# Kernel tuning notes

Hardware: AMD Instinct MI355X
Metric: run time of the kernel (lower is better)

Reference implementation:

```python
import jax, jax.numpy as jnp
import numpy as np

D_MODEL = 1024
VOCAB = 32000
NUM_HEADS = 3  # MTP steps
NHEAD = 2      # attention heads per encoder layer
D_FF = 2048    # torch TransformerEncoderLayer default dim_feedforward
EPS_RMS = 1e-8
EPS_LN = 1e-5


def rmsnorm(x):
    rms = jnp.sqrt(jnp.mean(x * x, axis=-1, keepdims=True) + EPS_RMS)
    return x / rms


def layernorm(x, g, b):
    m = jnp.mean(x, axis=-1, keepdims=True)
    v = jnp.mean((x - m) ** 2, axis=-1, keepdims=True)
    return (x - m) / jnp.sqrt(v + EPS_LN) * g + b


def encoder_layer_single_token(x, p):
    # x: (..., d). Self-attention over a length-1 sequence: softmax over one key
    # gives attention weight 1, so attn_out = Wo @ (Wv @ x). Post-norm (torch default).
    v = x @ p['Wv'].T + p['bv']
    attn = v @ p['Wo'].T + p['bo']
    x = layernorm(x + attn, p['ln1_g'], p['ln1_b'])
    ff = jax.nn.relu(x @ p['W1'].T + p['b1']) @ p['W2'].T + p['b2']
    x = layernorm(x + ff, p['ln2_g'], p['ln2_b'])
    return x


def setup_inputs() -> dict:
    key = jax.random.key(0)
    ks = jax.random.split(key, 4)
    token_ids = jax.random.randint(ks[0], (4, 512), 0, VOCAB)
    embed = jax.random.normal(ks[1], (VOCAB, D_MODEL), dtype=jnp.float32) * 0.02
    s = 1.0 / np.sqrt(D_MODEL)
    params = []
    kk = ks[2]
    for k in range(NUM_HEADS):
        kk, *sub = jax.random.split(kk, 10)
        p = {
            'Wmerge': jax.random.normal(sub[0], (D_MODEL, 2 * D_MODEL)) * s,
            'bmerge': jnp.zeros((D_MODEL,)),
            'Wv': jax.random.normal(sub[1], (D_MODEL, D_MODEL)) * s,
            'bv': jnp.zeros((D_MODEL,)),
            'Wo': jax.random.normal(sub[2], (D_MODEL, D_MODEL)) * s,
            'bo': jnp.zeros((D_MODEL,)),
            'W1': jax.random.normal(sub[3], (D_FF, D_MODEL)) * s,
            'b1': jnp.zeros((D_FF,)),
            'W2': jax.random.normal(sub[4], (D_MODEL, D_FF)) * (1.0 / np.sqrt(D_FF)),
            'b2': jnp.zeros((D_MODEL,)),
            'ln1_g': jnp.ones((D_MODEL,)), 'ln1_b': jnp.zeros((D_MODEL,)),
            'ln2_g': jnp.ones((D_MODEL,)), 'ln2_b': jnp.zeros((D_MODEL,)),
        }
        params.append(p)
    # flatten params into dict entries layer{k}_{name}
    out = {'token_ids': token_ids, 'embed': embed}
    for k, p in enumerate(params):
        for name, val in p.items():
            out[f'l{k}_{name}'] = val
    return out


def _forward(token_ids, embed, layers):
    B, T = token_ids.shape
    embeds = embed[token_ids]              # (B, T, d)
    n_pos = T - NUM_HEADS                  # positions i = 0 .. T-NUM_HEADS-1
    # vectorize over i: h_prev starts as h0_seq[:, i, :] for all i at once
    idx = jnp.arange(n_pos)
    h_prev = embeds[:, idx, :]             # (B, P, d)
    logits_list = []
    for k in range(NUM_HEADS):
        p = layers[k]
        tok = embeds[:, idx + (k + 1), :]  # (B, P, d) future token embeds
        merged = jnp.concatenate([rmsnorm(h_prev), rmsnorm(tok)], axis=-1)  # (B,P,2d)
        x = merged @ p['Wmerge'].T + p['bmerge']                            # (B,P,d)
        h_curr = encoder_layer_single_token(x, p)
        logits = h_curr @ embed.T          # tied unembed (B,P,V)
        logits_list.append(logits)
        h_prev = h_curr
    # stack -> (B, P, NUM_HEADS, V) matching torch stack(dim=1) per-position then outer list
    return jnp.stack(logits_list, axis=2)


def reference(token_ids, embed,
              l0_Wmerge, l0_bmerge, l0_Wv, l0_bv, l0_Wo, l0_bo, l0_W1, l0_b1, l0_W2, l0_b2, l0_ln1_g, l0_ln1_b, l0_ln2_g, l0_ln2_b,
              l1_Wmerge, l1_bmerge, l1_Wv, l1_bv, l1_Wo, l1_bo, l1_W1, l1_b1, l1_W2, l1_b2, l1_ln1_g, l1_ln1_b, l1_ln2_g, l1_ln2_b,
              l2_Wmerge, l2_bmerge, l2_Wv, l2_bv, l2_Wo, l2_bo, l2_W1, l2_b1, l2_W2, l2_b2, l2_ln1_g, l2_ln1_b, l2_ln2_g, l2_ln2_b):
    names = ['Wmerge', 'bmerge', 'Wv', 'bv', 'Wo', 'bo', 'W1', 'b1', 'W2', 'b2', 'ln1_g', 'ln1_b', 'ln2_g', 'ln2_b']
    vals = [l0_Wmerge, l0_bmerge, l0_Wv, l0_bv, l0_Wo, l0_bo, l0_W1, l0_b1, l0_W2, l0_b2, l0_ln1_g, l0_ln1_b, l0_ln2_g, l0_ln2_b,
            l1_Wmerge, l1_bmerge, l1_Wv, l1_bv, l1_Wo, l1_bo, l1_W1, l1_b1, l1_W2, l1_b2, l1_ln1_g, l1_ln1_b, l1_ln2_g, l1_ln2_b,
            l2_Wmerge, l2_bmerge, l2_Wv, l2_bv, l2_Wo, l2_bo, l2_W1, l2_b1, l2_W2, l2_b2, l2_ln1_g, l2_ln1_b, l2_ln2_g, l2_ln2_b]
    layers = [dict(zip(names, vals[i * 14:(i + 1) * 14])) for i in range(NUM_HEADS)]
    return _forward(token_ids, embed, layers)
```

## Files before the change

kernel.cpp:

```cpp
#include <hip/hip_runtime.h>


#define NPOS   509
#define MROWS  2036
#define MPAD   2048
#define DMODEL 1024

typedef _Float16 f16;
typedef _Float16 f16x8 __attribute__((ext_vector_type(8)));
typedef _Float16 f16x4 __attribute__((ext_vector_type(4)));
typedef float    f32x4 __attribute__((ext_vector_type(4)));

#define MFMA16(a, b, c) __builtin_amdgcn_mfma_f32_16x16x32_f16(a, b, c, 0, 0, 0)
#define VM0   asm volatile("s_waitcnt vmcnt(0)" ::: "memory")
#define VM2   asm volatile("s_waitcnt vmcnt(2)" ::: "memory")
#define VM4   asm volatile("s_waitcnt vmcnt(4)" ::: "memory")
#define LGKM0 asm volatile("s_waitcnt lgkmcnt(0)" ::: "memory")
#define SCHED0 __builtin_amdgcn_sched_barrier(0)
#define BAR   asm volatile("s_barrier" ::: "memory")

__device__ __forceinline__ void gld_lds16(const void* g, void* l) {
  __builtin_amdgcn_global_load_lds(
      (const __attribute__((address_space(1))) void*)g,
      (__attribute__((address_space(3))) void*)l, 16, 0, 0);
}

__global__ __launch_bounds__(256) void conv_f32_f16(const float* __restrict__ src,
                                                    f16* __restrict__ dst, long n) {
  long i = ((long)blockIdx.x * 256 + threadIdx.x) * 8;
  if (i + 8 <= n) {
    float4 a = *(const float4*)(src + i);
    float4 b = *(const float4*)(src + i + 4);
    f16x8 o = {(f16)a.x, (f16)a.y, (f16)a.z, (f16)a.w,
               (f16)b.x, (f16)b.y, (f16)b.z, (f16)b.w};
    *(f16x8*)(dst + i) = o;
  }
}

struct ConvArgs { const float* s[12]; f16* d[12]; long n[12]; };
__global__ __launch_bounds__(256) void conv_many(ConvArgs a) {
  int t = blockIdx.y;
  long i = ((long)blockIdx.x * 256 + threadIdx.x) * 8;
  if (i + 8 <= a.n[t]) {
    const float* src = a.s[t];
    float4 x = *(const float4*)(src + i);
    float4 y = *(const float4*)(src + i + 4);
    f16x8 o = {(f16)x.x, (f16)x.y, (f16)x.z, (f16)x.w,
               (f16)y.x, (f16)y.y, (f16)y.z, (f16)y.w};
    *(f16x8*)(a.d[t] + i) = o;
  }
}

struct TpArgs { const float* s[3]; f16* d[3]; };
__global__ __launch_bounds__(256) void transpose3(TpArgs a) {
  __shared__ float t[32][33];
  int h = blockIdx.z;
  int bx = blockIdx.x * 32, by = blockIdx.y * 32;
  int tx = threadIdx.x & 31, ty = threadIdx.x >> 5;
  const float* src = a.s[h];
  f16* dst = a.d[h];
  #pragma unroll
  for (int r = 0; r < 32; r += 8)
    t[ty + r][tx] = src[(long)(by + ty + r) * 1024 + bx + tx];
  __syncthreads();
  #pragma unroll
  for (int r = 0; r < 32; r += 8)
    dst[(long)(bx + ty + r) * 1024 + by + tx] = (f16)t[tx][ty + r];
}

struct BvoArgs { const float* Wo[3]; const float* bv[3]; const float* bo[3]; float* out[3]; };
__global__ __launch_bounds__(64) void make_bvo3(BvoArgs a) {
  int h = blockIdx.y, r = blockIdx.x, l = threadIdx.x;
  const float* Wo = a.Wo[h];
  const float* bv = a.bv[h];
  float s = 0.0f;
  for (int k = l; k < 1024; k += 64) s += Wo[(long)r * 1024 + k] * bv[k];
  #pragma unroll
  for (int off = 32; off > 0; off >>= 1) s += __shfl_xor(s, off);
  if (l == 0) a.out[h][r] = s + a.bo[h][r];
}

__device__ __forceinline__ float2 block_reduce2(float a, float b) {
  #pragma unroll
  for (int off = 32; off > 0; off >>= 1) {
    a += __shfl_xor(a, off);
    b += __shfl_xor(b, off);
  }
  __shared__ float2 red[4];
  int wv = threadIdx.x >> 6;
  if ((threadIdx.x & 63) == 0) red[wv] = make_float2(a, b);
  __syncthreads();
  float2 r0 = red[0], r1 = red[1], r2 = red[2], r3 = red[3];
  return make_float2(r0.x + r1.x + r2.x + r3.x, r0.y + r1.y + r2.y + r3.y);
}

__global__ __launch_bounds__(256) void merge_rms(const float* __restrict__ hprev,
                                                 const float* __restrict__ embed,
                                                 const int* __restrict__ tok,
                                                 f16* __restrict__ merged, int koff,
                                                 int hsel) {
  int r = blockIdx.x;
  int b = r / NPOS, t = r - b * NPOS;
  int tid = threadIdx.x;
  const float* hrow = (hsel >= 0)
      ? embed + (long)tok[b * 512 + t + hsel] * DMODEL
      : hprev + (long)r * DMODEL;
  float4 hv = ((const float4*)hrow)[tid];
  float4 tv = ((const float4*)(embed + (long)tok[b * 512 + t + koff] * DMODEL))[tid];
  float sh = hv.x * hv.x + hv.y * hv.y + hv.z * hv.z + hv.w * hv.w;
  float st = tv.x * tv.x + tv.y * tv.y + tv.z * tv.z + tv.w * tv.w;
  float2 tot = block_reduce2(sh, st);
  float ih = 1.0f / sqrtf(tot.x * (1.0f / DMODEL) + 1e-8f);
  float it = 1.0f / sqrtf(tot.y * (1.0f / DMODEL) + 1e-8f);
  f16x4 oh = {(f16)(hv.x * ih), (f16)(hv.y * ih), (f16)(hv.z * ih), (f16)(hv.w * ih)};
  f16x4 ot = {(f16)(tv.x * it), (f16)(tv.y * it), (f16)(tv.z * it), (f16)(tv.w * it)};
  *(f16x4*)(merged + (long)r * 2048 + tid * 4) = oh;
  *(f16x4*)(merged + (long)r * 2048 + 1024 + tid * 4) = ot;
}

__global__ __launch_bounds__(256) void add_ln(const float* __restrict__ x,
                                              const float* __restrict__ res,
                                              const float* __restrict__ g,
                                              const float* __restrict__ bb,
                                              float* __restrict__ yf,
                                              f16* __restrict__ yh) {
  int r = blockIdx.x, tid = threadIdx.x;
  float4 a = ((const float4*)(x + (long)r * DMODEL))[tid];
  float4 c = ((const float4*)(res + (long)r * DMODEL))[tid];
  a.x += c.x; a.y += c.y; a.z += c.z; a.w += c.w;
  float s  = a.x + a.y + a.z + a.w;
  float ss = a.x * a.x + a.y * a.y + a.z * a.z + a.w * a.w;
  float2 tot = block_reduce2(s, ss);
  float mean = tot.x * (1.0f / DMODEL);
  float var  = tot.y * (1.0f / DMODEL) - mean * mean;
  float inv  = 1.0f / sqrtf(var + 1e-5f);
  float4 gv = ((const float4*)g)[tid];
  float4 bv = ((const float4*)bb)[tid];
  float y0 = (a.x - mean) * inv * gv.x + bv.x;
  float y1 = (a.y - mean) * inv * gv.y + bv.y;
  float y2 = (a.z - mean) * inv * gv.z + bv.z;
  float y3 = (a.w - mean) * inv * gv.w + bv.w;
  float4 o = {y0, y1, y2, y3};
  ((float4*)(yf + (long)r * DMODEL))[tid] = o;
  f16x4 oh = {(f16)y0, (f16)y1, (f16)y2, (f16)y3};
  *(f16x4*)(yh + (long)r * DMODEL + tid * 4) = oh;
}

template <int HAS_BIAS, int RELU, int WF32, int WF16, int MASK>
__global__ __launch_bounds__(256) void gemm_sm(const f16* __restrict__ A,
                                               const f16* __restrict__ B,
                                               const float* __restrict__ bias,
                                               float* __restrict__ Cf,
                                               f16* __restrict__ Ch,
                                               int K, int N, long ldc, long coff,
                                               int mval, long zsA, long zsB, long zsC) {
  __shared__ __align__(16) f16 sA[3][2048];
  __shared__ __align__(16) f16 sB[3][2048];
  const int tid  = threadIdx.x;
  const int lane = tid & 63, wv = tid >> 6;
  const int wm = wv >> 1, wn = wv & 1;
  const int bm = blockIdx.y, bn = blockIdx.x;
  const int lr = lane & 15, lk = lane >> 4;

  A += (long)blockIdx.z * zsA;
  B += (long)blockIdx.z * zsB;
  Ch += (long)blockIdx.z * zsC;

  const f16* gA = A + ((long)(bm * 64 + (tid >> 2))) * K + (tid & 3) * 8;
  const f16* gB = B + ((long)(bn * 64 + (tid >> 2))) * K + (tid & 3) * 8;

  const int aoff = (wm * 32 + lr) * 32 + lk * 8;
  const int boff = (wn * 32 + lr) * 32 + lk * 8;

  f32x4 acc[2][2] = {};

#define SSTAGE(buf, kt)                                \
  gld_lds16(gA + (long)(kt) * 32, &sA[buf][tid * 8]);  \
  gld_lds16(gB + (long)(kt) * 32, &sB[buf][tid * 8]);

  const int nk = K >> 5;
  SSTAGE(0, 0);
  SSTAGE(1, 1);

  int cur = 0, stg = 2;
  for (int kt = 0; kt < nk; ++kt) {
    if (kt + 1 < nk) { VM2; } else { VM0; }
    BAR;
    if (kt + 2 < nk) { SSTAGE(stg, kt + 2); }
    f16x8 af0 = *(const f16x8*)&sA[cur][aoff];
    f16x8 af1 = *(const f16x8*)&sA[cur][aoff + 512];
    f16x8 bf0 = *(const f16x8*)&sB[cur][boff];
    f16x8 bf1 = *(const f16x8*)&sB[cur][boff + 512];
    acc[0][0] = MFMA16(af0, bf0, acc[0][0]);
    acc[0][1] = MFMA16(af0, bf1, acc[0][1]);
    acc[1][0] = MFMA16(af1, bf0, acc[1][0]);
    acc[1][1] = MFMA16(af1, bf1, acc[1][1]);
    cur = cur == 2 ? 0 : cur + 1;
    stg = stg == 2 ? 0 : stg + 1;
  }
#undef SSTAGE

  const int row0 = bm * 64 + wm * 32 + lk * 4;
  const int col0 = bn * 64 + wn * 32 + lr;
  #pragma unroll
  for (int mi = 0; mi < 2; ++mi) {
    #pragma unroll
    for (int ni = 0; ni < 2; ++ni) {
      int col = col0 + ni * 16;
      float bs = HAS_BIAS ? bias[col] : 0.0f;
      #pragma unroll
      for (int rg = 0; rg < 4; ++rg) {
        int row = row0 + mi * 16 + rg;
        if (!MASK || row < mval) {
          float v = acc[mi][ni][rg] + bs;
          if (RELU) v = v > 0.0f ? v : 0.0f;
          if (WF32) Cf[(long)row * ldc + coff + col] = v;
          if (WF16) Ch[(long)row * N + col] = (f16)v;
        }
      }
    }
  }
}

__global__ __launch_bounds__(512, 2) void gemm256x(const f16* __restrict__ A,
                                                   const f16* __restrict__ B,
                                                   float* __restrict__ C) {
  __shared__ __align__(16) f16 sA[2][2][8192];
  __shared__ __align__(16) f16 sB[2][2][8192];
  const int K = 1024;
  const int tid = threadIdx.x;
  const int lane = tid & 63;
  const int wv = tid >> 6;
  const int wm = wv >> 2, wn = wv & 3;
  const int lr = lane & 15, lk = lane >> 4;

  const int flat = blockIdx.y * 125 + blockIdx.x;
  const int xcd = flat & 7, idx = flat >> 3;
  const int bm = xcd * 3 + (idx % 3);
  const int bn = idx / 3;

  const int srow = tid >> 2;
  const int schunk = (tid & 3) ^ ((tid >> 3) & 3);
  const f16* gA = A + (long)(bm * 256 + srow) * K + schunk * 8;
  const f16* gB = B + (long)(bn * 256 + srow) * K + schunk * 8;
  const long rstep = 128L * (long)K;

  const int swz = ((lr >> 1) & 3) << 3;
  const int aoff = (((wm * 128 + lr) * 32) + lk * 8) ^ swz;
  const int boff = (((wn * 64  + lr) * 32) + lk * 8) ^ swz;

  f32x4 acc[8][4] = {};

#define STG_A(s, h, ko)                                                  \
  gld_lds16(gA + (ko) + (h) * 32, &sA[s][h][tid * 8]);                   \
  gld_lds16(gA + (ko) + (h) * 32 + rstep, &sA[s][h][tid * 8 + 4096]);
#define STG_B(s, h, ko)                                                  \
  gld_lds16(gB + (ko) + (h) * 32, &sB[s][h][tid * 8]);                   \
  gld_lds16(gB + (ko) + (h) * 32 + rstep, &sB[s][h][tid * 8 + 4096]);

  STG_A(0, 0, 0); STG_B(0, 0, 0); STG_A(0, 1, 0); STG_B(0, 1, 0);
  VM4;
  BAR;

  const int nt = 16;
  for (int t = 0; t < nt; ++t) {
    const int cur = t & 1, nxt = cur ^ 1;
    const long kn = (long)((t + 1 < nt) ? (t + 1) : 0) * 64;
    f16x8 alo[4], ahi[4], bf[4];

    #pragma unroll
    for (int i = 0; i < 4; ++i) alo[i] = *(const f16x8*)&sA[cur][0][aoff + i * 512];
    #pragma unroll
    for (int j = 0; j < 4; ++j) bf[j] = *(const f16x8*)&sB[cur][0][boff + j * 512];
    STG_A(nxt, 0, kn);
    BAR; LGKM0; SCHED0;
    __builtin_amdgcn_s_setprio(1);
    #pragma unroll
    for (int i = 0; i < 4; ++i)
      #pragma unroll
      for (int j = 0; j < 4; ++j)
        acc[i][j] = MFMA16(alo[i], bf[j], acc[i][j]);
    __builtin_amdgcn_s_setprio(0);
    BAR;

    #pragma unroll
    for (int i = 0; i < 4; ++i) ahi[i] = *(const f16x8*)&sA[cur][0][aoff + (i + 4) * 512];
    STG_B(nxt, 0, kn);
    VM4;
    BAR; LGKM0; SCHED0;
    __builtin_amdgcn_s_setprio(1);
    #pragma unroll
    for (int i = 0; i < 4; ++i)
      #pragma unroll
      for (int j = 0; j < 4; ++j)
        acc[i + 4][j] = MFMA16(ahi[i], bf[j], acc[i + 4][j]);
    __builtin_amdgcn_s_setprio(0);
    BAR;

    #pragma unroll
    for (int i = 0; i < 4; ++i) alo[i] = *(const f16x8*)&sA[cur][1][aoff + i * 512];
    #pragma unroll
    for (int j = 0; j < 4; ++j) bf[j] = *(const f16x8*)&sB[cur][1][boff + j * 512];
    STG_A(nxt, 1, kn);
    BAR; LGKM0; SCHED0;
    __builtin_amdgcn_s_setprio(1);
    #pragma unroll
    for (int i = 0; i < 4; ++i)
      #pragma unroll
      for (int j = 0; j < 4; ++j)
        acc[i][j] = MFMA16(alo[i], bf[j], acc[i][j]);
    __builtin_amdgcn_s_setprio(0);
    BAR;

    #pragma unroll
    for (int i = 0; i < 4; ++i) ahi[i] = *(const f16x8*)&sA[cur][1][aoff + (i + 4) * 512];
    STG_B(nxt, 1, kn);
    VM4;
    BAR; LGKM0; SCHED0;
    __builtin_amdgcn_s_setprio(1);
    #pragma unroll
    for (int i = 0; i < 4; ++i)
      #pragma unroll
      for (int j = 0; j < 4; ++j)
        acc[i + 4][j] = MFMA16(ahi[i], bf[j], acc[i + 4][j]);
    __builtin_amdgcn_s_setprio(0);
    BAR;
  }
  VM0;

  const int head = bm >> 3;
  const long coff = (long)head * 32000;
  const int row0 = (bm & 7) * 256 + wm * 128 + lk * 4;
  const int col0 = bn * 256 + wn * 64 + lr;
  #pragma unroll
  for (int mi = 0; mi < 8; ++mi) {
    #pragma unroll
    for (int ni = 0; ni < 4; ++ni) {
      int col = col0 + ni * 16;
      #pragma unroll
      for (int rg = 0; rg < 4; ++rg) {
        int row = row0 + mi * 16 + rg;
        if (row < MROWS) C[(long)row * 96000 + coff + col] = acc[mi][ni][rg];
      }
    }
  }
#undef STG_A
#undef STG_B
}

extern "C" void kernel_launch(void* const* d_in, const int* in_sizes, int n_in,
                              void* d_out, int out_size, void* d_ws, size_t ws_size,
                              hipStream_t stream) {
  const int*   tok   = (const int*)d_in[0];
  const float* embed = (const float*)d_in[1];
  auto P = [&](int k, int j) { return (const float*)d_in[2 + k * 14 + j]; };
  float* out = (float*)d_out;

  char* w = (char*)d_ws;
  auto alloc = [&](size_t bytes) { char* p = w; w += bytes; return p; };
  const size_t MM = (size_t)1024 * 1024;

  f16* embed_h = (f16*)alloc((size_t)32000 * 1024 * 2);
  f16* Wo_all  = (f16*)alloc(3 * MM * 2);
  f16* Wvo_all = (f16*)alloc(3 * MM * 2);
  f16 *Wm_h[3], *W1_h[3], *W2_h[3];
  for (int k = 0; k < 3; ++k) {
    Wm_h[k]  = (f16*)alloc((size_t)1024 * 2048 * 2);
    W1_h[k]  = (f16*)alloc((size_t)2048 * 1024 * 2);
    W2_h[k]  = (f16*)alloc((size_t)1024 * 2048 * 2);
  }
  float* hprev  = (float*)alloc((size_t)MPAD * 1024 * 4);
  f16*   h_all  = (f16*)alloc((size_t)3 * MPAD * 1024 * 2);
  f16*   merged = (f16*)alloc((size_t)MPAD * 2048 * 2);
  float* xf     = (float*)alloc((size_t)MPAD * 1024 * 4);
  f16*   xh     = (f16*)alloc((size_t)MPAD * 1024 * 2);
  f16*   ff1    = (f16*)alloc((size_t)MPAD * 2048 * 2);
  float* t1     = (float*)alloc((size_t)MPAD * 1024 * 4);
  float* bvo    = (float*)alloc(3 * 1024 * 4);
  f16* WvT_all = merged;

  conv_f32_f16<<<16000, 256, 0, stream>>>(embed, embed_h, (long)32000 * 1024);

  ConvArgs ca;
  for (int k = 0; k < 3; ++k) {
    ca.s[k*4+0] = P(k, 0); ca.d[k*4+0] = Wm_h[k];        ca.n[k*4+0] = (long)1024 * 2048;
    ca.s[k*4+1] = P(k, 4); ca.d[k*4+1] = Wo_all + k*MM;  ca.n[k*4+1] = (long)1024 * 1024;
    ca.s[k*4+2] = P(k, 6); ca.d[k*4+2] = W1_h[k];        ca.n[k*4+2] = (long)2048 * 1024;
    ca.s[k*4+3] = P(k, 8); ca.d[k*4+3] = W2_h[k];        ca.n[k*4+3] = (long)1024 * 2048;
  }
  conv_many<<<dim3(1024, 12), 256, 0, stream>>>(ca);

  TpArgs ta;
  for (int k = 0; k < 3; ++k) { ta.s[k] = P(k, 2); ta.d[k] = WvT_all + k * MM; }
  transpose3<<<dim3(32, 32, 3), 256, 0, stream>>>(ta);

  gemm_sm<0, 0, 0, 1, 0><<<dim3(16, 16, 3), 256, 0, stream>>>(
      Wo_all, WvT_all, nullptr, nullptr, Wvo_all, 1024, 1024, 1024L, 0L, 1024,
      (long)MM, (long)MM, (long)MM);

  BvoArgs ba;
  for (int k = 0; k < 3; ++k) {
    ba.Wo[k] = P(k, 4); ba.bv[k] = P(k, 3); ba.bo[k] = P(k, 5); ba.out[k] = bvo + k * 1024;
  }
  make_bvo3<<<dim3(1024, 3), 64, 0, stream>>>(ba);

  for (int k = 0; k < 3; ++k) {
    merge_rms<<<MROWS, 256, 0, stream>>>(hprev, embed, tok, merged, k + 1,
                                         k == 0 ? 0 : -1);
    gemm_sm<1, 0, 1, 1, 0><<<dim3(16, 32), 256, 0, stream>>>(
        merged, Wm_h[k], P(k, 1), xf, xh, 2048, 1024, 1024L, 0L, MROWS, 0L, 0L, 0L);
    gemm_sm<1, 0, 1, 0, 0><<<dim3(16, 32), 256, 0, stream>>>(
        xh, Wvo_all + k * MM, bvo + k * 1024, t1, nullptr, 1024, 1024, 1024L, 0L,
        MROWS, 0L, 0L, 0L);
    add_ln<<<MROWS, 256, 0, stream>>>(xf, t1, P(k, 10), P(k, 11), xf, xh);
    gemm_sm<1, 1, 0, 1, 0><<<dim3(32, 32), 256, 0, stream>>>(
        xh, W1_h[k], P(k, 7), nullptr, ff1, 1024, 2048, 2048L, 0L, MROWS, 0L, 0L, 0L);
    gemm_sm<1, 0, 1, 0, 0><<<dim3(16, 32), 256, 0, stream>>>(
        ff1, W2_h[k], P(k, 9), t1, nullptr, 2048, 1024, 1024L, 0L, MROWS, 0L, 0L, 0L);
    add_ln<<<MROWS, 256, 0, stream>>>(xf, t1, P(k, 12), P(k, 13), hprev,
                                      h_all + (size_t)k * MPAD * 1024);
  }

  gemm256x<<<dim3(125, 24), 512, 0, stream>>>(h_all, embed_h, out);
}
```

Baseline: 992.6 us.

## Restructure vocab GEMM to 256x128 tiles with 3-stage LDS pipeline

The final logits GEMM now uses 256-thread blocks computing 256x128 tiles instead of 512-thread 256x256 tiles, which doubles the grid. Each iteration covers a K-step of 32 and uses a triple-buffered LDS ring that prefetches two steps ahead with a vmcnt(6) wait, where before it used double buffering with a K-step of 64. The aim is to hide more global-load latency, cut barrier count per MFMA, and raise occupancy through smaller LDS use. The cost is that the smaller N tile re-reads A twice as often, and correctness depends on getting the new wait counts and slot rotation right.

```diff
diff --git a/kernel.cpp b/kernel.cpp
--- a/kernel.cpp
+++ b/kernel.cpp
@@ -14,7 +14,7 @@
 #define MFMA16(a, b, c) __builtin_amdgcn_mfma_f32_16x16x32_f16(a, b, c, 0, 0, 0)
 #define VM0   asm volatile("s_waitcnt vmcnt(0)" ::: "memory")
 #define VM2   asm volatile("s_waitcnt vmcnt(2)" ::: "memory")
-#define VM4   asm volatile("s_waitcnt vmcnt(4)" ::: "memory")
+#define VM6   asm volatile("s_waitcnt vmcnt(6)" ::: "memory")
 #define LGKM0 asm volatile("s_waitcnt lgkmcnt(0)" ::: "memory")
 #define SCHED0 __builtin_amdgcn_sched_barrier(0)
 #define BAR   asm volatile("s_barrier" ::: "memory")
@@ -222,19 +222,19 @@
   }
 }
 
-__global__ __launch_bounds__(512, 2) void gemm256x(const f16* __restrict__ A,
+__global__ __launch_bounds__(256, 2) void gemm256x(const f16* __restrict__ A,
                                                    const f16* __restrict__ B,
                                                    float* __restrict__ C) {
-  __shared__ __align__(16) f16 sA[2][2][8192];
-  __shared__ __align__(16) f16 sB[2][2][8192];
+  __shared__ __align__(16) f16 sA[3][8192];
+  __shared__ __align__(16) f16 sB[3][4096];
   const int K = 1024;
   const int tid = threadIdx.x;
   const int lane = tid & 63;
   const int wv = tid >> 6;
-  const int wm = wv >> 2, wn = wv & 3;
+  const int wm = wv >> 1, wn = wv & 1;
   const int lr = lane & 15, lk = lane >> 4;
 
-  const int flat = blockIdx.y * 125 + blockIdx.x;
+  const int flat = blockIdx.y * 250 + blockIdx.x;
   const int xcd = flat & 7, idx = flat >> 3;
   const int bm = xcd * 3 + (idx % 3);
   const int bn = idx / 3;
@@ -242,8 +242,7 @@
   const int srow = tid >> 2;
   const int schunk = (tid & 3) ^ ((tid >> 3) & 3);
   const f16* gA = A + (long)(bm * 256 + srow) * K + schunk * 8;
-  const f16* gB = B + (long)(bn * 256 + srow) * K + schunk * 8;
-  const long rstep = 128L * (long)K;
+  const f16* gB = B + (long)(bn * 128 + srow) * K + schunk * 8;
 
   const int swz = ((lr >> 1) & 3) << 3;
   const int aoff = (((wm * 128 + lr) * 32) + lk * 8) ^ swz;
@@ -251,29 +250,30 @@
 
   f32x4 acc[8][4] = {};
 
-#define STG_A(s, h, ko)                                                  \
-  gld_lds16(gA + (ko) + (h) * 32, &sA[s][h][tid * 8]);                   \
-  gld_lds16(gA + (ko) + (h) * 32 + rstep, &sA[s][h][tid * 8 + 4096]);
-#define STG_B(s, h, ko)                                                  \
-  gld_lds16(gB + (ko) + (h) * 32, &sB[s][h][tid * 8]);                   \
-  gld_lds16(gB + (ko) + (h) * 32 + rstep, &sB[s][h][tid * 8 + 4096]);
-
-  STG_A(0, 0, 0); STG_B(0, 0, 0); STG_A(0, 1, 0); STG_B(0, 1, 0);
-  VM4;
-  BAR;
-
-  const int nt = 16;
+#define STG_A(s, kt, i) gld_lds16(gA + (long)(kt) * 32 + (long)(i) * 64 * K, \
+                                  &sA[s][(i) * 2048 + tid * 8]);
+#define STG_B(s, kt, j) gld_lds16(gB + (long)(kt) * 32 + (long)(j) * 64 * K, \
+                                  &sB[s][(j) * 2048 + tid * 8]);
+#define STAGE_H1(s, kt) STG_A(s, kt, 0) STG_A(s, kt, 1) STG_B(s, kt, 0)
+#define STAGE_H2(s, kt) STG_A(s, kt, 2) STG_A(s, kt, 3) STG_B(s, kt, 1)
+
+  STAGE_H1(0, 0) STAGE_H2(0, 0)
+  STAGE_H1(1, 1) STAGE_H2(1, 1)
+  VM6; BAR;
+
+  const int nt = 32;
+  int slot = 0;
   for (int t = 0; t < nt; ++t) {
-    const int cur = t & 1, nxt = cur ^ 1;
-    const long kn = (long)((t + 1 < nt) ? (t + 1) : 0) * 64;
+    const int s2 = (slot >= 1) ? slot - 1 : slot + 2;
+    const int kt2 = (t + 2 < nt) ? (t + 2) : (t + 2 - nt);
     f16x8 alo[4], ahi[4], bf[4];
 
-    #pragma unroll
-    for (int i = 0; i < 4; ++i) alo[i] = *(const f16x8*)&sA[cur][0][aoff + i * 512];
-    #pragma unroll
-    for (int j = 0; j < 4; ++j) bf[j] = *(const f16x8*)&sB[cur][0][boff + j * 512];
-    STG_A(nxt, 0, kn);
-    BAR; LGKM0; SCHED0;
+    STAGE_H1(s2, kt2)
+    #pragma unroll
+    for (int i = 0; i < 4; ++i) alo[i] = *(const f16x8*)&sA[slot][aoff + i * 512];
+    #pragma unroll
+    for (int j = 0; j < 4; ++j) bf[j] = *(const f16x8*)&sB[slot][boff + j * 512];
+    LGKM0; SCHED0;
     __builtin_amdgcn_s_setprio(1);
     #pragma unroll
     for (int i = 0; i < 4; ++i)
@@ -283,11 +283,10 @@
     __builtin_amdgcn_s_setprio(0);
     BAR;
 
-    #pragma unroll
-    for (int i = 0; i < 4; ++i) ahi[i] = *(const f16x8*)&sA[cur][0][aoff + (i + 4) * 512];
-    STG_B(nxt, 0, kn);
-    VM4;
-    BAR; LGKM0; SCHED0;
+    STAGE_H2(s2, kt2)
+    #pragma unroll
+    for (int i = 0; i < 4; ++i) ahi[i] = *(const f16x8*)&sA[slot][aoff + (i + 4) * 512];
+    LGKM0; SCHED0;
     __builtin_amdgcn_s_setprio(1);
     #pragma unroll
     for (int i = 0; i < 4; ++i)
@@ -295,43 +294,17 @@
       for (int j = 0; j < 4; ++j)
         acc[i + 4][j] = MFMA16(ahi[i], bf[j], acc[i + 4][j]);
     __builtin_amdgcn_s_setprio(0);
+    VM6;
     BAR;
 
-    #pragma unroll
-    for (int i = 0; i < 4; ++i) alo[i] = *(const f16x8*)&sA[cur][1][aoff + i * 512];
-    #pragma unroll
-    for (int j = 0; j < 4; ++j) bf[j] = *(const f16x8*)&sB[cur][1][boff + j * 512];
-    STG_A(nxt, 1, kn);
-    BAR; LGKM0; SCHED0;
-    __builtin_amdgcn_s_setprio(1);
-    #pragma unroll
-    for (int i = 0; i < 4; ++i)
-      #pragma unroll
-      for (int j = 0; j < 4; ++j)
-        acc[i][j] = MFMA16(alo[i], bf[j], acc[i][j]);
-    __builtin_amdgcn_s_setprio(0);
-    BAR;
-
-    #pragma unroll
-    for (int i = 0; i < 4; ++i) ahi[i] = *(const f16x8*)&sA[cur][1][aoff + (i + 4) * 512];
-    STG_B(nxt, 1, kn);
-    VM4;
-    BAR; LGKM0; SCHED0;
-    __builtin_amdgcn_s_setprio(1);
-    #pragma unroll
-    for (int i = 0; i < 4; ++i)
-      #pragma unroll
-      for (int j = 0; j < 4; ++j)
-        acc[i + 4][j] = MFMA16(ahi[i], bf[j], acc[i + 4][j]);
-    __builtin_amdgcn_s_setprio(0);
-    BAR;
+    slot = (slot == 2) ? 0 : slot + 1;
   }
   VM0;
 
   const int head = bm >> 3;
   const long coff = (long)head * 32000;
   const int row0 = (bm & 7) * 256 + wm * 128 + lk * 4;
-  const int col0 = bn * 256 + wn * 64 + lr;
+  const int col0 = bn * 128 + wn * 64 + lr;
   #pragma unroll
   for (int mi = 0; mi < 8; ++mi) {
     #pragma unroll
@@ -346,6 +319,8 @@
   }
 #undef STG_A
 #undef STG_B
+#undef STAGE_H1
+#undef STAGE_H2
 }
 
 extern "C" void kernel_launch(void* const* d_in, const int* in_sizes, int n_in,
@@ -421,5 +396,5 @@
                                       h_all + (size_t)k * MPAD * 1024);
   }
 
-  gemm256x<<<dim3(125, 24), 512, 0, stream>>>(h_all, embed_h, out);
-}
+  gemm256x<<<dim3(250, 24), 256, 0, stream>>>(h_all, embed_h, out);
+}
```

Result: slower. 1.112 ms (+12.0%).
